# Optimization experiments

Measured on AMD Instinct MI355X. Metric: run time of the kernel, lower is better.

Reference implementation:

```python
import jax, jax.numpy as jnp
import numpy as np

WS = 8                       # window size (square)
N = WS * WS                  # tokens per window
RES_H, RES_W = 32, 32        # input_resolution
DIM = 512
NUM_HEADS = 16
HEAD_DIM = DIM // NUM_HEADS
SCALE = HEAD_DIM ** -0.5
TABLE = 2 * WS - 1           # size of a_p/b_p/a_r/b_r tables
B_ = 1024                    # num_windows * batch


def _rel_coords():
    c = np.arange(WS)
    coords = np.stack(np.meshgrid(c, c, indexing='ij'))          # (2, WS, WS)
    cf = coords.reshape(2, -1)                                   # (2, N)
    rel = cf[:, :, None] - cf[:, None, :]                        # (2, N, N), values in [-(WS-1), WS-1]
    return rel[0], rel[1]                                        # radius (dh), azimuth (dw)

RADIUS_NP, AZIMUTH_NP = _rel_coords()
# torch indexes the (2*WS-1)-row tables with negative indices -> python wrap: -k maps to TABLE-k
IDX_R = jnp.asarray(RADIUS_NP % TABLE)
IDX_AZ = jnp.asarray(AZIMUTH_NP % TABLE)
RADIUS = jnp.asarray(RADIUS_NP, dtype=jnp.float32)               # (N, N)
AZIMUTH = jnp.asarray(AZIMUTH_NP, dtype=jnp.float32)             # (N, N)


def setup_inputs() -> dict:
    key = jax.random.key(0)
    ks = jax.random.split(key, 10)
    return {
        'x': jax.random.normal(ks[0], (B_, N, DIM), dtype=jnp.float32),
        'theta_max': jnp.ones((), dtype=jnp.float32) * 1.5708,   # ~pi/2 field-of-view half-angle
        'qkv_w': jax.random.normal(ks[1], (3 * DIM, DIM), dtype=jnp.float32) * 0.02,
        'qkv_b': jnp.zeros((3 * DIM,), dtype=jnp.float32),
        'proj_w': jax.random.normal(ks[2], (DIM, DIM), dtype=jnp.float32) * 0.02,
        'proj_b': jnp.zeros((DIM,), dtype=jnp.float32),
        'a_p': jax.random.normal(ks[3], (TABLE, NUM_HEADS), dtype=jnp.float32) * 0.02,
        'b_p': jax.random.normal(ks[4], (TABLE, NUM_HEADS), dtype=jnp.float32) * 0.02,
        'a_r': jax.random.normal(ks[5], (TABLE, NUM_HEADS), dtype=jnp.float32) * 0.02,
        'b_r': jax.random.normal(ks[6], (TABLE, NUM_HEADS), dtype=jnp.float32) * 0.02,
    }


def _trig_bias(table_a, table_b, idx, angle):
    # table_[ab]: (TABLE, H); idx: (N, N) int; angle: (N, N) float (possibly traced)
    a = table_a[idx]                                              # (N, N, H)
    b = table_b[idx]
    ang = angle[:, :, None]                                       # (N, N, 1)
    bias = a * jnp.cos(ang) + b * jnp.sin(ang)                    # (N, N, H)
    return jnp.transpose(bias, (2, 0, 1))                         # (H, N, N)


def reference(x, theta_max, qkv_w, qkv_b, proj_w, proj_b, a_p, b_p, a_r, b_r):
    Bw, n, c = x.shape
    qkv = x @ qkv_w.T + qkv_b                                     # (B_, N, 3*DIM)
    qkv = qkv.reshape(Bw, n, 3, NUM_HEADS, HEAD_DIM)
    qkv = jnp.transpose(qkv, (2, 0, 3, 1, 4))                     # (3, B_, H, N, hd)
    q, k, v = qkv[0] * SCALE, qkv[1], qkv[2]

    attn = jnp.einsum('bhid,bhjd->bhij', q, k)                    # (B_, H, N, N)

    az_angle = AZIMUTH * (2.0 * np.pi / RES_W)                    # (N, N)
    A_phi = _trig_bias(a_p, b_p, IDX_AZ, az_angle)                # (H, N, N)
    r_angle = RADIUS * (theta_max / RES_H)                        # (N, N), traced via theta_max
    A_theta = _trig_bias(a_r, b_r, IDX_R, r_angle)                # (H, N, N)

    attn = attn + A_phi[None] + A_theta[None]
    attn = jax.nn.softmax(attn, axis=-1)

    out = jnp.einsum('bhij,bhjd->bhid', attn, v)                  # (B_, H, N, hd)
    out = jnp.transpose(out, (0, 2, 1, 3)).reshape(Bw, n, c)      # (B_, N, DIM)
    out = out @ proj_w.T + proj_b
    return out
```

## Files before the change

### kernel.cpp

```cpp
#include <hip/hip_runtime.h>
#include <hip/hip_bf16.h>


typedef __bf16 bf16_t;
typedef bf16_t bf16x8 __attribute__((ext_vector_type(8)));
typedef float  f32x4  __attribute__((ext_vector_type(4)));

#define NWIN   1024
#define NTOK   64
#define DIM    512
#define NHEADS 16
#define HD     32
#define MTOT   (NWIN*NTOK)
#define QKVN   (3*DIM)
#define SCALE  0.17677669529663687f

__device__ __forceinline__ void async_copy16(const void* g, void* lds_generic) {
    __builtin_amdgcn_global_load_lds(
        (__attribute__((address_space(1))) unsigned int*)(unsigned long long)g,
        (__attribute__((address_space(3))) unsigned int*)(unsigned int)(unsigned long long)lds_generic,
        16, 0, 0);
}

__global__ void cvt_f32_bf16(const float* __restrict__ in, bf16_t* __restrict__ out, int n8) {
    int i = blockIdx.x * blockDim.x + threadIdx.x;
    if (i >= n8) return;
    const float4* p = (const float4*)in;
    float4 a = p[2*i], b = p[2*i+1];
    bf16x8 o;
    o[0]=(bf16_t)a.x; o[1]=(bf16_t)a.y; o[2]=(bf16_t)a.z; o[3]=(bf16_t)a.w;
    o[4]=(bf16_t)b.x; o[5]=(bf16_t)b.y; o[6]=(bf16_t)b.z; o[7]=(bf16_t)b.w;
    ((bf16x8*)out)[i] = o;
}

__global__ void bias_kernel(const float* __restrict__ ap, const float* __restrict__ bp,
                            const float* __restrict__ ar, const float* __restrict__ br,
                            const float* __restrict__ theta_max, float* __restrict__ bias) {
    int idx = blockIdx.x * 256 + threadIdx.x;
    int h  = idx >> 12;
    int ij = idx & 4095;
    int i = ij >> 6, j = ij & 63;
    int ri = i >> 3, ci = i & 7, rj = j >> 3, cj = j & 7;
    int rad = ri - rj, az = ci - cj;
    int idx_r  = rad < 0 ? rad + 15 : rad;
    int idx_az = az  < 0 ? az  + 15 : az;
    float azang = (float)az * 0.19634954084936207f;
    float rang  = (float)rad * (theta_max[0] * (1.0f/32.0f));
    float v = ap[idx_az*NHEADS + h] * cosf(azang) + bp[idx_az*NHEADS + h] * sinf(azang)
            + ar[idx_r *NHEADS + h] * cosf(rang)  + br[idx_r *NHEADS + h] * sinf(rang);
    bias[idx] = v;
}

template<int OUT_BF16>
__global__ __launch_bounds__(256, 2)
void gemm_bt(const bf16_t* __restrict__ A, const bf16_t* __restrict__ Bt,
             const float* __restrict__ bias, void* __restrict__ C,
             int M, int N, int K, int ntiles) {
    __shared__ bf16_t sA[128*64];
    __shared__ bf16_t sB[128*64];

    int bid = blockIdx.x;
    int bm = bid / ntiles, bn = bid % ntiles;
    int tid = threadIdx.x;
    int w = tid >> 6, lane = tid & 63;
    int quad = lane >> 4, l16 = lane & 15;
    int wm = w >> 1, wn = w & 1;

    f32x4 acc[4][4] = {};

    const bf16_t* Abase = A  + (size_t)(bm*128) * K;
    const bf16_t* Bbase = Bt + (size_t)(bn*128) * K;

    for (int k0 = 0; k0 < K; k0 += 64) {
        for (int i = 0; i < 4; ++i) {
            int off = w*4096 + i*1024 + lane*16;
            int r  = off >> 7;
            int pb = (off >> 4) & 7;
            int cb = pb ^ (r & 7);
            async_copy16(Abase + (size_t)r*K + k0 + cb*8, (char*)sA + w*4096 + i*1024);
            async_copy16(Bbase + (size_t)r*K + k0 + cb*8, (char*)sB + w*4096 + i*1024);
        }
        __syncthreads();

        for (int kk = 0; kk < 64; kk += 32) {
            bf16x8 af[4], bf[4];
            for (int mi = 0; mi < 4; ++mi) {
                int r  = wm*64 + mi*16 + l16;
                int cb = (kk >> 3) + quad;
                int pb = cb ^ (r & 7);
                af[mi] = *(const bf16x8*)((const char*)sA + r*128 + pb*16);
            }
            for (int ni = 0; ni < 4; ++ni) {
                int r  = wn*64 + ni*16 + l16;
                int cb = (kk >> 3) + quad;
                int pb = cb ^ (r & 7);
                bf[ni] = *(const bf16x8*)((const char*)sB + r*128 + pb*16);
            }
            for (int mi = 0; mi < 4; ++mi)
                for (int ni = 0; ni < 4; ++ni)
                    acc[mi][ni] = __builtin_amdgcn_mfma_f32_16x16x32_bf16(
                        af[mi], bf[ni], acc[mi][ni], 0, 0, 0);
        }
        __syncthreads();
    }

    for (int ni = 0; ni < 4; ++ni) {
        int col = bn*128 + wn*64 + ni*16 + l16;
        float bv = bias[col];
        for (int mi = 0; mi < 4; ++mi) {
            int row0 = bm*128 + wm*64 + mi*16 + quad*4;
            f32x4 a = acc[mi][ni];
            for (int reg = 0; reg < 4; ++reg) {
                float v = a[reg] + bv;
                size_t o = (size_t)(row0 + reg) * N + col;
                if (OUT_BF16) ((bf16_t*)C)[o] = (bf16_t)v;
                else          ((float*)C)[o]  = v;
            }
        }
    }
}

__global__ __launch_bounds__(256, 2)
void attn_proj_kernel(const bf16_t* __restrict__ qkv, const float* __restrict__ bias,
                      const bf16_t* __restrict__ projw, const float* __restrict__ projb,
                      float* __restrict__ out) {
    __shared__ bf16_t aout[32768];
    __shared__ bf16_t pbuf[4][512];

    int b = blockIdx.x;
    int tid = threadIdx.x;
    int w = tid >> 6, lane = tid & 63, quad = lane >> 4, l16 = lane & 15;
    const bf16_t* base = qkv + (size_t)(b*64) * QKVN;
    f32x4 zero = {0.f, 0.f, 0.f, 0.f};

    #pragma unroll 1
    for (int t = 0; t < 4; ++t) {
        int h = w*4 + t;

        bf16x8 ak[4], bq[4];
        #pragma unroll
        for (int jt = 0; jt < 4; ++jt)
            ak[jt] = *(const bf16x8*)(base + (size_t)(jt*16 + l16)*QKVN + 512 + h*32 + quad*8);
        #pragma unroll
        for (int it = 0; it < 4; ++it)
            bq[it] = *(const bf16x8*)(base + (size_t)(it*16 + l16)*QKVN + h*32 + quad*8);

        bf16x8 av[2][2];
        #pragma unroll
        for (int dt = 0; dt < 2; ++dt)
            #pragma unroll
            for (int ks = 0; ks < 2; ++ks) {
                const bf16_t* vb = base + (size_t)(ks*32 + quad*8)*QKVN + 1024 + h*32 + dt*16 + l16;
                bf16x8 tmp;
                #pragma unroll
                for (int e = 0; e < 8; ++e) tmp[e] = vb[(size_t)e*QKVN];
                av[dt][ks] = tmp;
            }

        f32x4 st[4][4];
        #pragma unroll
        for (int jt = 0; jt < 4; ++jt)
            #pragma unroll
            for (int it = 0; it < 4; ++it)
                st[jt][it] = __builtin_amdgcn_mfma_f32_16x16x32_bf16(ak[jt], bq[it], zero, 0, 0, 0);

        const float* bh = bias + h*4096;
        float p[4][4][4];
        #pragma unroll
        for (int it = 0; it < 4; ++it)
            #pragma unroll
            for (int jt = 0; jt < 4; ++jt) {
                float4 b4 = *(const float4*)(bh + (it*16 + l16)*64 + jt*16 + quad*4);
                p[jt][it][0] = st[jt][it][0]*SCALE + b4.x;
                p[jt][it][1] = st[jt][it][1]*SCALE + b4.y;
                p[jt][it][2] = st[jt][it][2]*SCALE + b4.z;
                p[jt][it][3] = st[jt][it][3]*SCALE + b4.w;
            }

        float inv[4];
        #pragma unroll
        for (int it = 0; it < 4; ++it) {
            float m = p[0][it][0];
            #pragma unroll
            for (int jt = 0; jt < 4; ++jt)
                #pragma unroll
                for (int r = 0; r < 4; ++r) m = fmaxf(m, p[jt][it][r]);
            m = fmaxf(m, __shfl_xor(m, 16));
            m = fmaxf(m, __shfl_xor(m, 32));
            float s = 0.f;
            #pragma unroll
            for (int jt = 0; jt < 4; ++jt)
                #pragma unroll
                for (int r = 0; r < 4; ++r) {
                    p[jt][it][r] = __expf(p[jt][it][r] - m);
                    s += p[jt][it][r];
                }
            s += __shfl_xor(s, 16);
            s += __shfl_xor(s, 32);
            inv[it] = 1.0f / s;
        }

        f32x4 accO[2][4];
        #pragma unroll
        for (int ks = 0; ks < 2; ++ks)
            #pragma unroll
            for (int it = 0; it < 4; ++it) {
                #pragma unroll
                for (int jh = 0; jh < 2; ++jh) {
                    int jt = ks*2 + jh;
                    #pragma unroll
                    for (int r = 0; r < 4; ++r) {
                        int jloc = jh*16 + quad*4 + r;
                        pbuf[w][((jloc >> 3)*16 + l16)*8 + (jloc & 7)] = (bf16_t)p[jt][it][r];
                    }
                }
                bf16x8 bp = ((const bf16x8*)pbuf[w])[lane];
                if (ks == 0) {
                    accO[0][it] = __builtin_amdgcn_mfma_f32_16x16x32_bf16(av[0][0], bp, zero, 0, 0, 0);
                    accO[1][it] = __builtin_amdgcn_mfma_f32_16x16x32_bf16(av[1][0], bp, zero, 0, 0, 0);
                } else {
                    accO[0][it] = __builtin_amdgcn_mfma_f32_16x16x32_bf16(av[0][1], bp, accO[0][it], 0, 0, 0);
                    accO[1][it] = __builtin_amdgcn_mfma_f32_16x16x32_bf16(av[1][1], bp, accO[1][it], 0, 0, 0);
                }
            }

        #pragma unroll
        for (int dt = 0; dt < 2; ++dt)
            #pragma unroll
            for (int it = 0; it < 4; ++it) {
                #pragma unroll
                for (int r = 0; r < 4; ++r) {
                    int d = dt*16 + quad*4 + r;
                    aout[(it*16 + h)*512 + ((d >> 3)*16 + l16)*8 + (d & 7)] =
                        (bf16_t)(accO[dt][it][r] * inv[it]);
                }
            }
    }

    __syncthreads();

    #pragma unroll 1
    for (int half = 0; half < 2; ++half) {
        f32x4 acc[4][4] = {};
        #pragma unroll 1
        for (int hk = 0; hk < 16; ++hk) {
            bf16x8 af[4], bw[4];
            #pragma unroll
            for (int mi = 0; mi < 4; ++mi)
                af[mi] = ((const bf16x8*)(aout + (mi*16 + hk)*512))[lane];
            #pragma unroll
            for (int ni = 0; ni < 4; ++ni)
                bw[ni] = *(const bf16x8*)(projw + (size_t)(w*128 + half*64 + ni*16 + l16)*512 + hk*32 + quad*8);
            #pragma unroll
            for (int mi = 0; mi < 4; ++mi)
                #pragma unroll
                for (int ni = 0; ni < 4; ++ni)
                    acc[mi][ni] = __builtin_amdgcn_mfma_f32_16x16x32_bf16(af[mi], bw[ni], acc[mi][ni], 0, 0, 0);
        }
        #pragma unroll
        for (int ni = 0; ni < 4; ++ni) {
            int col = w*128 + half*64 + ni*16 + l16;
            float bv = projb[col];
            #pragma unroll
            for (int mi = 0; mi < 4; ++mi) {
                int row0 = b*64 + mi*16 + quad*4;
                f32x4 a = acc[mi][ni];
                #pragma unroll
                for (int reg = 0; reg < 4; ++reg)
                    out[(size_t)(row0 + reg)*DIM + col] = a[reg] + bv;
            }
        }
    }
}

extern "C" void kernel_launch(void* const* d_in, const int* in_sizes, int n_in,
                              void* d_out, int out_size, void* d_ws, size_t ws_size,
                              hipStream_t stream) {
    const float* x      = (const float*)d_in[0];
    const float* theta  = (const float*)d_in[1];
    const float* qkv_w  = (const float*)d_in[2];
    const float* qkv_b  = (const float*)d_in[3];
    const float* proj_w = (const float*)d_in[4];
    const float* proj_b = (const float*)d_in[5];
    const float* a_p    = (const float*)d_in[6];
    const float* b_p    = (const float*)d_in[7];
    const float* a_r    = (const float*)d_in[8];
    const float* b_r    = (const float*)d_in[9];
    float* out = (float*)d_out;

    char* ws = (char*)d_ws;
    bf16_t* qkvbuf = (bf16_t*)ws;
    bf16_t* xb     = (bf16_t*)(ws + 201326592);
    bf16_t* wqkv   = (bf16_t*)(ws + 201326592 + 67108864);
    bf16_t* wproj  = (bf16_t*)(ws + 201326592 + 67108864 + 1572864);
    float*  biasbf = (float*) (ws + 201326592 + 67108864 + 1572864 + 524288);

    cvt_f32_bf16<<<(MTOT*DIM/8)/256, 256, 0, stream>>>(x, xb, MTOT*DIM/8);
    cvt_f32_bf16<<<(QKVN*DIM/8)/256, 256, 0, stream>>>(qkv_w, wqkv, QKVN*DIM/8);
    cvt_f32_bf16<<<(DIM*DIM/8)/256, 256, 0, stream>>>(proj_w, wproj, DIM*DIM/8);

    bias_kernel<<<256, 256, 0, stream>>>(a_p, b_p, a_r, b_r, theta, biasbf);

    gemm_bt<1><<<(MTOT/128)*(QKVN/128), 256, 0, stream>>>(xb, wqkv, qkv_b, qkvbuf,
                                                          MTOT, QKVN, DIM, QKVN/128);
    attn_proj_kernel<<<NWIN, 256, 0, stream>>>(qkvbuf, biasbf, wproj, proj_b, out);
}
```

Baseline: 521.5 us.

## Pipeline per-head loads, drop softmax max pass, use exp2 and vectorized LDS stores

Restructures the attention stage so each wave prefetches the next head's Q/K/V registers while computing the current head, and double-buffers the projection GEMM operand loads. Softmax drops the row-max subtraction and uses hardware exp2 with log2(e) folded into the scale and precomputed bias. The P and output tiles are written to LDS as packed 4-element vectors instead of scalars. This removes a reduction pass and exposed memory latency but raises register pressure and risks overflow if scores are large.

New measurement: 517.0 us. Within noise of the previous version (-0.9%).

```diff
diff --git a/kernel.cpp b/kernel.cpp
--- a/kernel.cpp
+++ b/kernel.cpp
@@ -3,6 +3,7 @@
 
 
 typedef __bf16 bf16_t;
+typedef bf16_t bf16x4 __attribute__((ext_vector_type(4)));
 typedef bf16_t bf16x8 __attribute__((ext_vector_type(8)));
 typedef float  f32x4  __attribute__((ext_vector_type(4)));
 
@@ -13,7 +14,7 @@
 #define HD     32
 #define MTOT   (NWIN*NTOK)
 #define QKVN   (3*DIM)
-#define SCALE  0.17677669529663687f
+#define SCLG2E 0.25503494f
 
 __device__ __forceinline__ void async_copy16(const void* g, void* lds_generic) {
     __builtin_amdgcn_global_load_lds(
@@ -48,7 +49,7 @@
     float rang  = (float)rad * (theta_max[0] * (1.0f/32.0f));
     float v = ap[idx_az*NHEADS + h] * cosf(azang) + bp[idx_az*NHEADS + h] * sinf(azang)
             + ar[idx_r *NHEADS + h] * cosf(rang)  + br[idx_r *NHEADS + h] * sinf(rang);
-    bias[idx] = v;
+    bias[idx] = v * 1.4426950408889634f;
 }
 
 template<int OUT_BF16>
@@ -125,27 +126,23 @@
                       const bf16_t* __restrict__ projw, const float* __restrict__ projb,
                       float* __restrict__ out) {
     __shared__ bf16_t aout[32768];
-    __shared__ bf16_t pbuf[4][512];
+    __shared__ bf16_t pbuf[4][2048];
 
     int b = blockIdx.x;
     int tid = threadIdx.x;
     int w = tid >> 6, lane = tid & 63, quad = lane >> 4, l16 = lane & 15;
+    int qh = quad >> 1, ql = quad & 1;
     const bf16_t* base = qkv + (size_t)(b*64) * QKVN;
     f32x4 zero = {0.f, 0.f, 0.f, 0.f};
-
-    #pragma unroll 1
-    for (int t = 0; t < 4; ++t) {
-        int h = w*4 + t;
-
-        bf16x8 ak[4], bq[4];
+    bf16_t* pb = pbuf[w];
+
+    auto LOADH = [&](int h, bf16x8* ak, bf16x8* bq, bf16x8* av) {
         #pragma unroll
         for (int jt = 0; jt < 4; ++jt)
             ak[jt] = *(const bf16x8*)(base + (size_t)(jt*16 + l16)*QKVN + 512 + h*32 + quad*8);
         #pragma unroll
         for (int it = 0; it < 4; ++it)
             bq[it] = *(const bf16x8*)(base + (size_t)(it*16 + l16)*QKVN + h*32 + quad*8);
-
-        bf16x8 av[2][2];
         #pragma unroll
         for (int dt = 0; dt < 2; ++dt)
             #pragma unroll
@@ -154,109 +151,116 @@
                 bf16x8 tmp;
                 #pragma unroll
                 for (int e = 0; e < 8; ++e) tmp[e] = vb[(size_t)e*QKVN];
-                av[dt][ks] = tmp;
-            }
-
-        f32x4 st[4][4];
-        #pragma unroll
-        for (int jt = 0; jt < 4; ++jt)
+                av[dt*2+ks] = tmp;
+            }
+    };
+
+    auto DOHEAD = [&](int h, bf16x8* ak, bf16x8* bq, bf16x8* av) {
+        const float* bh = bias + h*4096;
+        f32x4 accO[2][4];
+        float s[4];
+        #pragma unroll
+        for (int it = 0; it < 4; ++it) { s[it] = 0.f; accO[0][it] = zero; accO[1][it] = zero; }
+
+        #pragma unroll
+        for (int ks = 0; ks < 2; ++ks) {
+            f32x4 bb[2][4];
+            #pragma unroll
+            for (int jh = 0; jh < 2; ++jh)
+                #pragma unroll
+                for (int it = 0; it < 4; ++it)
+                    bb[jh][it] = *(const f32x4*)(bh + (it*16 + l16)*64 + (ks*2+jh)*16 + quad*4);
+
+            f32x4 st[2][4];
+            #pragma unroll
+            for (int jh = 0; jh < 2; ++jh)
+                #pragma unroll
+                for (int it = 0; it < 4; ++it)
+                    st[jh][it] = __builtin_amdgcn_mfma_f32_16x16x32_bf16(ak[ks*2+jh], bq[it], zero, 0, 0, 0);
+
             #pragma unroll
             for (int it = 0; it < 4; ++it)
-                st[jt][it] = __builtin_amdgcn_mfma_f32_16x16x32_bf16(ak[jt], bq[it], zero, 0, 0, 0);
-
-        const float* bh = bias + h*4096;
-        float p[4][4][4];
-        #pragma unroll
-        for (int it = 0; it < 4; ++it)
-            #pragma unroll
-            for (int jt = 0; jt < 4; ++jt) {
-                float4 b4 = *(const float4*)(bh + (it*16 + l16)*64 + jt*16 + quad*4);
-                p[jt][it][0] = st[jt][it][0]*SCALE + b4.x;
-                p[jt][it][1] = st[jt][it][1]*SCALE + b4.y;
-                p[jt][it][2] = st[jt][it][2]*SCALE + b4.z;
-                p[jt][it][3] = st[jt][it][3]*SCALE + b4.w;
-            }
-
-        float inv[4];
+                #pragma unroll
+                for (int jh = 0; jh < 2; ++jh) {
+                    float e0 = __builtin_amdgcn_exp2f(st[jh][it][0]*SCLG2E + bb[jh][it][0]);
+                    float e1 = __builtin_amdgcn_exp2f(st[jh][it][1]*SCLG2E + bb[jh][it][1]);
+                    float e2 = __builtin_amdgcn_exp2f(st[jh][it][2]*SCLG2E + bb[jh][it][2]);
+                    float e3 = __builtin_amdgcn_exp2f(st[jh][it][3]*SCLG2E + bb[jh][it][3]);
+                    s[it] += (e0 + e1) + (e2 + e3);
+                    bf16x4 pk4;
+                    pk4[0] = (bf16_t)e0; pk4[1] = (bf16_t)e1;
+                    pk4[2] = (bf16_t)e2; pk4[3] = (bf16_t)e3;
+                    *(bf16x4*)(pb + it*512 + (2*jh + qh)*128 + l16*8 + ql*4) = pk4;
+                }
+
+            #pragma unroll
+            for (int it = 0; it < 4; ++it) {
+                bf16x8 bp = ((const bf16x8*)(pb + it*512))[lane];
+                accO[0][it] = __builtin_amdgcn_mfma_f32_16x16x32_bf16(av[0*2+ks], bp, accO[0][it], 0, 0, 0);
+                accO[1][it] = __builtin_amdgcn_mfma_f32_16x16x32_bf16(av[1*2+ks], bp, accO[1][it], 0, 0, 0);
+            }
+        }
+
         #pragma unroll
         for (int it = 0; it < 4; ++it) {
-            float m = p[0][it][0];
-            #pragma unroll
-            for (int jt = 0; jt < 4; ++jt)
-                #pragma unroll
-                for (int r = 0; r < 4; ++r) m = fmaxf(m, p[jt][it][r]);
-            m = fmaxf(m, __shfl_xor(m, 16));
-            m = fmaxf(m, __shfl_xor(m, 32));
-            float s = 0.f;
-            #pragma unroll
-            for (int jt = 0; jt < 4; ++jt)
-                #pragma unroll
-                for (int r = 0; r < 4; ++r) {
-                    p[jt][it][r] = __expf(p[jt][it][r] - m);
-                    s += p[jt][it][r];
-                }
-            s += __shfl_xor(s, 16);
-            s += __shfl_xor(s, 32);
-            inv[it] = 1.0f / s;
-        }
-
-        f32x4 accO[2][4];
-        #pragma unroll
-        for (int ks = 0; ks < 2; ++ks)
-            #pragma unroll
-            for (int it = 0; it < 4; ++it) {
-                #pragma unroll
-                for (int jh = 0; jh < 2; ++jh) {
-                    int jt = ks*2 + jh;
-                    #pragma unroll
-                    for (int r = 0; r < 4; ++r) {
-                        int jloc = jh*16 + quad*4 + r;
-                        pbuf[w][((jloc >> 3)*16 + l16)*8 + (jloc & 7)] = (bf16_t)p[jt][it][r];
-                    }
-                }
-                bf16x8 bp = ((const bf16x8*)pbuf[w])[lane];
-                if (ks == 0) {
-                    accO[0][it] = __builtin_amdgcn_mfma_f32_16x16x32_bf16(av[0][0], bp, zero, 0, 0, 0);
-                    accO[1][it] = __builtin_amdgcn_mfma_f32_16x16x32_bf16(av[1][0], bp, zero, 0, 0, 0);
-                } else {
-                    accO[0][it] = __builtin_amdgcn_mfma_f32_16x16x32_bf16(av[0][1], bp, accO[0][it], 0, 0, 0);
-                    accO[1][it] = __builtin_amdgcn_mfma_f32_16x16x32_bf16(av[1][1], bp, accO[1][it], 0, 0, 0);
-                }
-            }
-
-        #pragma unroll
-        for (int dt = 0; dt < 2; ++dt)
-            #pragma unroll
-            for (int it = 0; it < 4; ++it) {
-                #pragma unroll
-                for (int r = 0; r < 4; ++r) {
-                    int d = dt*16 + quad*4 + r;
-                    aout[(it*16 + h)*512 + ((d >> 3)*16 + l16)*8 + (d & 7)] =
-                        (bf16_t)(accO[dt][it][r] * inv[it]);
-                }
-            }
-    }
+            float sv = s[it];
+            sv += __shfl_xor(sv, 16);
+            sv += __shfl_xor(sv, 32);
+            float inv = __builtin_amdgcn_rcpf(sv);
+            #pragma unroll
+            for (int dt = 0; dt < 2; ++dt) {
+                bf16x4 o4;
+                #pragma unroll
+                for (int r = 0; r < 4; ++r) o4[r] = (bf16_t)(accO[dt][it][r] * inv);
+                *(bf16x4*)(aout + (it*16 + h)*512 + (2*dt + qh)*128 + l16*8 + ql*4) = o4;
+            }
+        }
+    };
+
+    bf16x8 akA[4], bqA[4], avA[4], akB[4], bqB[4], avB[4];
+    int h0 = w*4;
+    LOADH(h0+0, akA, bqA, avA);
+    LOADH(h0+1, akB, bqB, avB);
+    DOHEAD(h0+0, akA, bqA, avA);
+    LOADH(h0+2, akA, bqA, avA);
+    DOHEAD(h0+1, akB, bqB, avB);
+    LOADH(h0+3, akB, bqB, avB);
+    DOHEAD(h0+2, akA, bqA, avA);
+    DOHEAD(h0+3, akB, bqB, avB);
 
     __syncthreads();
 
     #pragma unroll 1
     for (int half = 0; half < 2; ++half) {
         f32x4 acc[4][4] = {};
-        #pragma unroll 1
-        for (int hk = 0; hk < 16; ++hk) {
-            bf16x8 af[4], bw[4];
+        const bf16_t* wb = projw + (size_t)(w*128 + half*64 + l16)*512 + quad*8;
+
+        bf16x8 af0[4], bw0[4], af1[4], bw1[4];
+        auto LD = [&](bf16x8* af, bf16x8* bw, int hk) {
             #pragma unroll
             for (int mi = 0; mi < 4; ++mi)
                 af[mi] = ((const bf16x8*)(aout + (mi*16 + hk)*512))[lane];
             #pragma unroll
             for (int ni = 0; ni < 4; ++ni)
-                bw[ni] = *(const bf16x8*)(projw + (size_t)(w*128 + half*64 + ni*16 + l16)*512 + hk*32 + quad*8);
+                bw[ni] = *(const bf16x8*)(wb + (size_t)(ni*16)*512 + hk*32);
+        };
+        auto MM = [&](bf16x8* af, bf16x8* bw) {
             #pragma unroll
             for (int mi = 0; mi < 4; ++mi)
                 #pragma unroll
                 for (int ni = 0; ni < 4; ++ni)
                     acc[mi][ni] = __builtin_amdgcn_mfma_f32_16x16x32_bf16(af[mi], bw[ni], acc[mi][ni], 0, 0, 0);
-        }
+        };
+
+        LD(af0, bw0, 0);
+        #pragma unroll 1
+        for (int hk = 0; hk < 16; hk += 2) {
+            LD(af1, bw1, hk+1);
+            MM(af0, bw0);
+            if (hk + 2 < 16) LD(af0, bw0, hk+2);
+            MM(af1, bw1);
+        }
+
         #pragma unroll
         for (int ni = 0; ni < 4; ++ni) {
             int col = w*128 + half*64 + ni*16 + l16;
```
